# Optimization experiments

Hardware: AMD Instinct MI355X
Metric: run time of the kernel (lower is better)

Reference implementation:

```python
import jax, jax.numpy as jnp
import numpy as np

NUM_HEADS = 32
ROPE_BASE = 10000.0
MASK_NEG = -66504.0  # from (1 - tril) * -66504.0 in the source


def _rotate_half(x):
    d = x.shape[-1] // 2
    return jnp.concatenate([-x[..., d:], x[..., :d]], axis=-1)


def setup_inputs() -> dict:
    key = jax.random.key(0)
    k1, k2, k3, k4 = jax.random.split(key, 4)
    S, B, E = 2048, 2, 2048
    return {
        "hidden_states": jax.random.normal(k1, (S, B, E), dtype=jnp.float32) * 0.02,
        "qkv_w": jax.random.normal(k2, (E, 3 * E), dtype=jnp.float32) * 0.02,
        "qkv_b": jax.random.normal(k3, (3 * E,), dtype=jnp.float32) * 0.02,
        "out_w": jax.random.normal(k4, (E, E), dtype=jnp.float32) * 0.02,
        "out_b": jnp.zeros((E,), dtype=jnp.float32),
    }


def reference(hidden_states, qkv_w, qkv_b, out_w, out_b):
    # seq-first prompt/prefill path of IPEXTransformerAtten
    S, B, E = hidden_states.shape
    H = NUM_HEADS
    D = E // H

    # fused QKV projection (mm_qkv_out)
    qkv = jnp.einsum('sbe,ef->sbf', hidden_states, qkv_w) + qkv_b  # [S,B,3E]
    q, k, v = jnp.split(qkv, 3, axis=-1)
    q = q.reshape(S, B, H, D)
    k = k.reshape(S, B, H, D)
    v = v.reshape(S, B, H, D)

    # rotary embedding (GPT-NeoX style, full head_dim)
    inv_freq = 1.0 / (ROPE_BASE ** (jnp.arange(0, D, 2, dtype=jnp.float32) / D))
    freqs = jnp.arange(S, dtype=jnp.float32)[:, None] * inv_freq  # [S, D/2]
    emb = jnp.concatenate([freqs, freqs], axis=-1)  # [S, D]
    cos = jnp.cos(emb)[:, None, None, :].astype(hidden_states.dtype)
    sin = jnp.sin(emb)[:, None, None, :].astype(hidden_states.dtype)
    q = q * cos + _rotate_half(q) * sin
    k = k * cos + _rotate_half(k) * sin

    # scaled dot-product attention with causal mask
    scale = 1.0 / jnp.sqrt(jnp.array(D, dtype=hidden_states.dtype))
    scores = jnp.einsum('sbhd,tbhd->bhst', q, k) * scale  # [B,H,S,S]
    causal = jnp.tril(jnp.ones((S, S), dtype=scores.dtype))
    scores = scores + (1.0 - causal) * MASK_NEG
    attn = jax.nn.softmax(scores, axis=-1)
    ctx = jnp.einsum('bhst,tbhd->sbhd', attn, v).reshape(S, B, E)

    # output projection
    return jnp.einsum('sbe,ef->sbf', ctx, out_w) + out_b
```

## Files before the change

kernel.cpp:

```cpp
#include <hip/hip_runtime.h>
#include <hip/hip_bf16.h>

#define S_LEN 2048
#define BATCH 2
#define EMB   2048
#define NH    32
#define HD    64
#define M_ROWS (S_LEN * BATCH)
#define QKV_N  (3 * EMB)

typedef short bf16x8 __attribute__((ext_vector_type(8)));
typedef float f32x4  __attribute__((ext_vector_type(4)));

__device__ __forceinline__ unsigned short f2bf(float f) {
  unsigned int u = __float_as_uint(f);
  u += 0x7fffu + ((u >> 16) & 1u);
  return (unsigned short)(u >> 16);
}
__device__ __forceinline__ unsigned int pkbf(float a, float b) {
  __hip_bfloat162 t = __float22bfloat162_rn(float2{a, b});
  return *reinterpret_cast<unsigned int*>(&t);
}
__device__ __forceinline__ void async_copy16(const void* g, void* lds) {
  __builtin_amdgcn_global_load_lds(
      (const __attribute__((address_space(1))) void*)g,
      (__attribute__((address_space(3))) void*)lds, 16, 0, 0);
}

#if __has_builtin(__builtin_amdgcn_exp2f)
#define EXP2F(x) __builtin_amdgcn_exp2f(x)
#else
#define EXP2F(x) __expf((x) * 0.6931471805599453f)
#endif


__global__ __launch_bounds__(256) void cast_to_bf16(
    const float* __restrict__ in, unsigned short* __restrict__ out, int n4) {
  int i = blockIdx.x * 256 + threadIdx.x;
  if (i >= n4) return;
  float4 v = reinterpret_cast<const float4*>(in)[i];
  ushort4 o;
  o.x = f2bf(v.x); o.y = f2bf(v.y); o.z = f2bf(v.z); o.w = f2bf(v.w);
  reinterpret_cast<ushort4*>(out)[i] = o;
}

__global__ __launch_bounds__(256) void transpose_cast2(
    const float* __restrict__ qkv_w, const float* __restrict__ out_w,
    unsigned short* __restrict__ qkvwT, unsigned short* __restrict__ outwT) {
  __shared__ float tile[32][33];
  const int z = blockIdx.z;
  const int C = z ? EMB : QKV_N;
  const int bc = blockIdx.x * 32;
  if (bc >= C) return;
  const float* in = z ? out_w : qkv_w;
  unsigned short* out = z ? outwT : qkvwT;
  const int br = blockIdx.y * 32;
  const int tx = threadIdx.x & 31, ty = threadIdx.x >> 5;
  #pragma unroll
  for (int rr = ty; rr < 32; rr += 8)
    tile[rr][tx] = in[(size_t)(br + rr) * C + bc + tx];
  __syncthreads();
  #pragma unroll
  for (int rr = ty; rr < 32; rr += 8)
    out[(size_t)(bc + rr) * EMB + br + tx] = f2bf(tile[tx][rr]);
}


__global__ __launch_bounds__(256) void gemm_qkv(
    const unsigned short* __restrict__ A,
    const unsigned short* __restrict__ Wt,
    const float* __restrict__ bias,
    unsigned short* __restrict__ Qo,
    unsigned short* __restrict__ Ko,
    unsigned short* __restrict__ Vo) {
  __shared__ __align__(16) unsigned short As[128 * 64];
  __shared__ __align__(16) unsigned short Bs[128 * 64];
  const int tid = threadIdx.x;
  const int n0 = blockIdx.x * 128;
  const int m0 = blockIdx.y * 128;
  const int wave = tid >> 6, lane = tid & 63;
  const int wm = (wave >> 1) * 64, wn = (wave & 1) * 64;
  const int lm = lane & 15, lq = lane >> 4;
  const int K = 2048;

  const int srow = tid >> 3;
  const int gch  = (tid & 7) ^ (srow & 7);
  const unsigned short* Ab = A  + (size_t)(m0 + srow) * K + gch * 8;
  const unsigned short* Bb = Wt + (size_t)(n0 + srow) * K + gch * 8;

  f32x4 acc[4][4] = {};

  for (int k0 = 0; k0 < K; k0 += 64) {
    #pragma unroll
    for (int rep = 0; rep < 4; rep++) {
      async_copy16(Ab + (size_t)rep * 32 * K + k0, As + (size_t)(tid + 256 * rep) * 8);
      async_copy16(Bb + (size_t)rep * 32 * K + k0, Bs + (size_t)(tid + 256 * rep) * 8);
    }
    __syncthreads();
    #pragma unroll
    for (int ks = 0; ks < 2; ks++) {
      bf16x8 a[4], b[4];
      #pragma unroll
      for (int i = 0; i < 4; i++) {
        const int R = wm + i*16 + lm;
        a[i] = *reinterpret_cast<const bf16x8*>(
            As + (size_t)R * 64 + (((ks*4 + lq) ^ (R & 7)) * 8));
      }
      #pragma unroll
      for (int j = 0; j < 4; j++) {
        const int R = wn + j*16 + lm;
        b[j] = *reinterpret_cast<const bf16x8*>(
            Bs + (size_t)R * 64 + (((ks*4 + lq) ^ (R & 7)) * 8));
      }
      #pragma unroll
      for (int i = 0; i < 4; i++)
        #pragma unroll
        for (int j = 0; j < 4; j++)
          acc[i][j] = __builtin_amdgcn_mfma_f32_16x16x32_bf16(a[i], b[j], acc[i][j], 0, 0, 0);
    }
    __syncthreads();
  }

  const int which = n0 >> 11;
  unsigned short* dst = (which == 0) ? Qo : (which == 1) ? Ko : Vo;
  float bv[4];
  #pragma unroll
  for (int j = 0; j < 4; j++) bv[j] = bias[n0 + wn + j*16 + lm];

  if (which < 2) {
    const float osc = (which == 0) ? 0.18033688011112042f : 1.0f;
    #pragma unroll
    for (int j = 0; j < 2; j++) {
      const int n = n0 + wn + j*16 + lm;
      const int e = n & (EMB - 1), h = e >> 6, d = e & 63;
      const float invf = EXP2F((float)d * -0.4152410118609203f);
      #pragma unroll
      for (int i = 0; i < 4; i++) {
        #pragma unroll
        for (int r = 0; r < 4; r++) {
          const int m = m0 + wm + i*16 + lq*4 + r;
          const int s = m >> 1, b = m & 1;
          const float v1 = acc[i][j][r]   + bv[j];
          const float v2 = acc[i][j+2][r] + bv[j+2];
          float sn, cs;
          __sincosf((float)s * invf, &sn, &cs);
          const size_t base = (((size_t)b * NH + h) * S_LEN + s) * HD + d;
          dst[base]      = f2bf((v1 * cs - v2 * sn) * osc);
          dst[base + 32] = f2bf((v2 * cs + v1 * sn) * osc);
        }
      }
    }
  } else {
    #pragma unroll
    for (int j = 0; j < 4; j++) {
      const int n = n0 + wn + j*16 + lm;
      const int e = n & (EMB - 1), h = e >> 6, d = e & 63;
      #pragma unroll
      for (int i = 0; i < 4; i++) {
        #pragma unroll
        for (int r = 0; r < 4; r++) {
          const int m = m0 + wm + i*16 + lq*4 + r;
          const int s = m >> 1, b = m & 1;
          dst[(((size_t)b * NH + h) * S_LEN + s) * HD + d] = f2bf(acc[i][j][r] + bv[j]);
        }
      }
    }
  }
}


__global__ __launch_bounds__(256) void transpose_v(
    const unsigned short* __restrict__ V, unsigned short* __restrict__ VT) {
  __shared__ unsigned short t[64][65];
  const int bh = blockIdx.y;
  const int s0 = blockIdx.x * 64;
  const int tx = threadIdx.x & 63, ty = threadIdx.x >> 6;
  const unsigned short* src = V + ((size_t)bh * S_LEN + s0) * HD;
  #pragma unroll
  for (int r = ty; r < 64; r += 4)
    t[r][tx] = src[(size_t)r * HD + tx];
  __syncthreads();
  unsigned short* dst = VT + (size_t)bh * HD * S_LEN + s0;
  #pragma unroll
  for (int r = ty; r < 64; r += 4)
    dst[(size_t)r * S_LEN + tx] = t[tx][r];
}


__global__ __launch_bounds__(256) void attn_kernel(
    const unsigned short* __restrict__ Q,
    const unsigned short* __restrict__ K,
    const unsigned short* __restrict__ VT,
    unsigned short* __restrict__ ctx) {
  const int bh = blockIdx.x;
  const int p  = blockIdx.y;
  const int tid = threadIdx.x;
  const int wave = tid >> 6, lane = tid & 63;
  const int lm = lane & 15, lq = lane >> 4;
  const int b = bh >> 5, h = bh & 31;
  const char* Qb8 = (const char*)(Q  + (size_t)bh * S_LEN * HD);
  const char* Kb8 = (const char*)(K  + (size_t)bh * S_LEN * HD);
  const char* Vb8 = (const char*)(VT + (size_t)bh * HD * S_LEN);

  __shared__ __align__(16) unsigned short Ks[2][2][64][32];
  __shared__ __align__(16) unsigned short Vs[2][2][64][32];

  const int rA = p * 128 + wave * 32;
  const int rB = (15 - p) * 128 + wave * 32;
  const int nt = ((15 - p) * 128 >> 6) + 2;

  const int srw = tid >> 2, sc16 = (tid & 3) * 16;

  bf16x8 qf[2][2][2];
  #pragma unroll
  for (int s = 0; s < 2; s++) {
    const int rr = s ? rB : rA;
    #pragma unroll
    for (int i = 0; i < 2; i++)
      #pragma unroll
      for (int ks = 0; ks < 2; ks++)
        qf[s][i][ks] = *reinterpret_cast<const bf16x8*>(
            Qb8 + (size_t)(rr + i*16 + lm) * 128 + ks*64 + lq*16);
  }

  f32x4 O[2][2][4] = {};
  float l[2][2] = {};

  {
    char* kd = (char*)&Ks[0][0][0][0];
    char* vd = (char*)&Vs[0][0][0][0];
    async_copy16(Kb8 + (size_t)srw * 128      + sc16, kd        + tid*16);
    async_copy16(Kb8 + (size_t)srw * 128 + 64 + sc16, kd + 4096 + tid*16);
    async_copy16(Vb8 + (size_t)srw * 4096      + sc16, vd        + tid*16);
    async_copy16(Vb8 + (size_t)srw * 4096 + 64 + sc16, vd + 4096 + tid*16);
  }
  __syncthreads();

  for (int t = 0; t < nt; t++) {
    const int t0 = t * 64;
    const int buf = t & 1;

    if (t + 1 < nt) {
      const int t1 = t0 + 64;
      char* kd = (char*)&Ks[buf ^ 1][0][0][0];
      char* vd = (char*)&Vs[buf ^ 1][0][0][0];
      async_copy16(Kb8 + (size_t)(t1 + srw) * 128      + sc16, kd        + tid*16);
      async_copy16(Kb8 + (size_t)(t1 + srw) * 128 + 64 + sc16, kd + 4096 + tid*16);
      async_copy16(Vb8 + (size_t)srw * 4096 + t1*2      + sc16, vd        + tid*16);
      async_copy16(Vb8 + (size_t)srw * 4096 + t1*2 + 64 + sc16, vd + 4096 + tid*16);
    }

    const char* KsB = (const char*)&Ks[buf][0][0][0];
    const char* VsB = (const char*)&Vs[buf][0][0][0];

    #pragma unroll
    for (int s = 0; s < 2; s++) {
      const int rr = s ? rB : rA;
      if (t0 <= rr + 31) {
        const bool clean = (t0 + 63 <= rr);
        int jm[2];
        jm[1] = clean ? 4 : (((rr + 31 - t0) >> 4) + 1);
        jm[0] = clean ? 4 : ((t0 > rr + 15) ? 0 : (((rr + 15 - t0) >> 4) + 1));

        f32x4 sc[2][4] = {};
        #pragma unroll
        for (int ks = 0; ks < 2; ks++) {
          bf16x8 kf[4];
          #pragma unroll
          for (int j = 0; j < 4; j++)
            if (j < jm[1])
              kf[j] = *reinterpret_cast<const bf16x8*>(
                  KsB + ks*4096 + (j*16 + lm)*64 + lq*16);
          #pragma unroll
          for (int i = 0; i < 2; i++)
            #pragma unroll
            for (int j = 0; j < 4; j++)
              if (j < jm[i])
                sc[i][j] = __builtin_amdgcn_mfma_f32_16x16x32_bf16(
                    kf[j], qf[s][i][ks], sc[i][j], 0, 0, 0);
        }

        unsigned int pb[2][2][4];
        #pragma unroll
        for (int i = 0; i < 2; i++) {
          #pragma unroll
          for (int j = 0; j < 4; j++) {
            const int w = j >> 1, rbase = (j & 1) * 2;
            if (j < jm[i]) {
              const bool full = clean || (t0 + j*16 + 15 <= rr + i*16);
              float pe[4];
              #pragma unroll
              for (int r = 0; r < 4; r++) {
                float v = EXP2F(sc[i][j][r]);
                if (!full) {
                  const int tt = t0 + j*16 + lq*4 + r;
                  const int mm = rr + i*16 + lm;
                  v = (tt <= mm) ? v : 0.0f;
                }
                pe[r] = v;
              }
              l[s][i] += (pe[0] + pe[1]) + (pe[2] + pe[3]);
              pb[i][w][rbase]     = pkbf(pe[0], pe[1]);
              pb[i][w][rbase + 1] = pkbf(pe[2], pe[3]);
            } else {
              pb[i][w][rbase] = 0; pb[i][w][rbase + 1] = 0;
            }
          }
        }

        #pragma unroll
        for (int w = 0; w < 2; w++) {
          if (t0 + w*32 <= rr + 31) {
            bf16x8 av[4];
            #pragma unroll
            for (int jj = 0; jj < 4; jj++) {
              const char* vrow = VsB + w*4096 + (jj*16 + lm)*64;
              unsigned long long q0 = *reinterpret_cast<const unsigned long long*>(vrow + lq*8);
              unsigned long long q1 = *reinterpret_cast<const unsigned long long*>(vrow + 32 + lq*8);
              union { unsigned long long q[2]; bf16x8 v; } u;
              u.q[0] = q0; u.q[1] = q1;
              av[jj] = u.v;
            }
            #pragma unroll
            for (int i = 0; i < 2; i++) {
              if (jm[i] > w*2) {
                union { unsigned int u[4]; bf16x8 v; } pu;
                pu.u[0] = pb[i][w][0]; pu.u[1] = pb[i][w][1];
                pu.u[2] = pb[i][w][2]; pu.u[3] = pb[i][w][3];
                #pragma unroll
                for (int jj = 0; jj < 4; jj++)
                  O[s][i][jj] = __builtin_amdgcn_mfma_f32_16x16x32_bf16(
                      av[jj], pu.v, O[s][i][jj], 0, 0, 0);
              }
            }
          }
        }
      }
    }
    __syncthreads();
  }

  #pragma unroll
  for (int s = 0; s < 2; s++) {
    const int rr = s ? rB : rA;
    #pragma unroll
    for (int i = 0; i < 2; i++) {
      float sum = l[s][i];
      sum += __shfl_xor(sum, 16, 64);
      sum += __shfl_xor(sum, 32, 64);
      const float inv = 1.0f / sum;
      const int srow = rr + i*16 + lm;
      #pragma unroll
      for (int jj = 0; jj < 4; jj++) {
        uint2 e;
        e.x = pkbf(O[s][i][jj][0] * inv, O[s][i][jj][1] * inv);
        e.y = pkbf(O[s][i][jj][2] * inv, O[s][i][jj][3] * inv);
        *reinterpret_cast<uint2*>(
            ctx + ((size_t)srow * BATCH + b) * EMB + h*HD + jj*16 + lq*4) = e;
      }
    }
  }
}


__global__ __launch_bounds__(256) void gemm_out(
    const unsigned short* __restrict__ A,
    const unsigned short* __restrict__ Wt,
    const float* __restrict__ bias,
    float* __restrict__ out) {
  __shared__ __align__(16) unsigned short As[2][128 * 64];
  __shared__ __align__(16) unsigned short Bs[2][128 * 64];
  const int tid = threadIdx.x;
  const int n0 = blockIdx.x * 128;
  const int m0 = blockIdx.y * 128;
  const int wave = tid >> 6, lane = tid & 63;
  const int wm = (wave >> 1) * 64, wn = (wave & 1) * 64;
  const int lm = lane & 15, lq = lane >> 4;
  const int K = 2048;

  const int srow = tid >> 3;
  const int gch  = (tid & 7) ^ (srow & 7);
  const unsigned short* Ab = A  + (size_t)(m0 + srow) * K + gch * 8;
  const unsigned short* Bb = Wt + (size_t)(n0 + srow) * K + gch * 8;

  f32x4 acc[4][4] = {};

  #pragma unroll
  for (int rep = 0; rep < 4; rep++) {
    async_copy16(Ab + (size_t)rep * 32 * K, As[0] + (size_t)(tid + 256 * rep) * 8);
    async_copy16(Bb + (size_t)rep * 32 * K, Bs[0] + (size_t)(tid + 256 * rep) * 8);
  }
  __syncthreads();

  for (int kt = 0; kt < 32; kt++) {
    const int buf = kt & 1;
    if (kt + 1 < 32) {
      const int k1 = (kt + 1) * 64;
      #pragma unroll
      for (int rep = 0; rep < 4; rep++) {
        async_copy16(Ab + (size_t)rep * 32 * K + k1, As[buf ^ 1] + (size_t)(tid + 256 * rep) * 8);
        async_copy16(Bb + (size_t)rep * 32 * K + k1, Bs[buf ^ 1] + (size_t)(tid + 256 * rep) * 8);
      }
    }
    #pragma unroll
    for (int ks = 0; ks < 2; ks++) {
      bf16x8 a[4], b[4];
      #pragma unroll
      for (int i = 0; i < 4; i++) {
        const int R = wm + i*16 + lm;
        a[i] = *reinterpret_cast<const bf16x8*>(
            As[buf] + (size_t)R * 64 + (((ks*4 + lq) ^ (R & 7)) * 8));
      }
      #pragma unroll
      for (int j = 0; j < 4; j++) {
        const int R = wn + j*16 + lm;
        b[j] = *reinterpret_cast<const bf16x8*>(
            Bs[buf] + (size_t)R * 64 + (((ks*4 + lq) ^ (R & 7)) * 8));
      }
      #pragma unroll
      for (int i = 0; i < 4; i++)
        #pragma unroll
        for (int j = 0; j < 4; j++)
          acc[i][j] = __builtin_amdgcn_mfma_f32_16x16x32_bf16(a[i], b[j], acc[i][j], 0, 0, 0);
    }
    __syncthreads();
  }

  #pragma unroll
  for (int j = 0; j < 4; j++) {
    const int n = n0 + wn + j*16 + lm;
    const float bv = bias[n];
    #pragma unroll
    for (int i = 0; i < 4; i++) {
      #pragma unroll
      for (int r = 0; r < 4; r++) {
        const int m = m0 + wm + i*16 + lq*4 + r;
        out[(size_t)m * EMB + n] = acc[i][j][r] + bv;
      }
    }
  }
}


extern "C" void kernel_launch(void* const* d_in, const int* in_sizes, int n_in,
                              void* d_out, int out_size, void* d_ws, size_t ws_size,
                              hipStream_t stream) {
  const float* hidden = (const float*)d_in[0];
  const float* qkv_w  = (const float*)d_in[1];
  const float* qkv_b  = (const float*)d_in[2];
  const float* out_w  = (const float*)d_in[3];
  const float* out_b  = (const float*)d_in[4];
  float* out = (float*)d_out;

  unsigned short* ws = (unsigned short*)d_ws;
  unsigned short* hbf   = ws;
  unsigned short* qkvwT = hbf   + (size_t)M_ROWS * EMB;
  unsigned short* outwT = qkvwT + (size_t)QKV_N * EMB;
  unsigned short* Qb    = outwT + (size_t)EMB * EMB;
  unsigned short* Kb    = Qb    + (size_t)64 * S_LEN * HD;
  unsigned short* Vb    = Kb    + (size_t)64 * S_LEN * HD;
  unsigned short* VTb   = Vb    + (size_t)64 * S_LEN * HD;
  unsigned short* ctx   = VTb   + (size_t)64 * S_LEN * HD;

  cast_to_bf16<<<(M_ROWS * EMB / 4) / 256, 256, 0, stream>>>(hidden, hbf, M_ROWS * EMB / 4);
  transpose_cast2<<<dim3(QKV_N / 32, EMB / 32, 2), 256, 0, stream>>>(qkv_w, out_w, qkvwT, outwT);

  gemm_qkv<<<dim3(QKV_N / 128, M_ROWS / 128), 256, 0, stream>>>(hbf, qkvwT, qkv_b, Qb, Kb, Vb);

  transpose_v<<<dim3(S_LEN / 64, 64), 256, 0, stream>>>(Vb, VTb);

  attn_kernel<<<dim3(64, 8), 256, 0, stream>>>(Qb, Kb, VTb, ctx);

  gemm_out<<<dim3(EMB / 128, M_ROWS / 128), 256, 0, stream>>>(ctx, outwT, out_b, out);
}
```

Baseline: 414.2 us.

## Split attention into one-strip blocks, swizzle V in LDS, single-buffer gemm_out

The attention kernel previously paired a short and a long causal query strip in each block for load balance. Now each block handles one strip, with twice as many blocks launched and the longest strips scheduled first. V tiles are XOR-swizzled when copied into LDS, and the read path applies the matching swizzle, to reduce bank conflicts. The output GEMM drops double buffering to cut LDS use, which may raise occupancy but loses overlap of loads with compute. The weight transpose grid is flattened so no blocks launch only to exit early.

```diff
diff --git a/kernel.cpp b/kernel.cpp
--- a/kernel.cpp
+++ b/kernel.cpp
@@ -48,12 +48,12 @@
     const float* __restrict__ qkv_w, const float* __restrict__ out_w,
     unsigned short* __restrict__ qkvwT, unsigned short* __restrict__ outwT) {
   __shared__ float tile[32][33];
-  const int z = blockIdx.z;
-  const int C = z ? EMB : QKV_N;
-  const int bc = blockIdx.x * 32;
-  if (bc >= C) return;
-  const float* in = z ? out_w : qkv_w;
-  unsigned short* out = z ? outwT : qkvwT;
+  const int bx = blockIdx.x;
+  const float* in;
+  unsigned short* out;
+  int C, bc;
+  if (bx < 192) { in = qkv_w; out = qkvwT; C = QKV_N; bc = bx * 32; }
+  else          { in = out_w; out = outwT; C = EMB;   bc = (bx - 192) * 32; }
   const int br = blockIdx.y * 32;
   const int tx = threadIdx.x & 31, ty = threadIdx.x >> 5;
   #pragma unroll
@@ -193,7 +193,7 @@
     const unsigned short* __restrict__ VT,
     unsigned short* __restrict__ ctx) {
   const int bh = blockIdx.x;
-  const int p  = blockIdx.y;
+  const int strip = 15 - blockIdx.y;
   const int tid = threadIdx.x;
   const int wave = tid >> 6, lane = tid & 63;
   const int lm = lane & 15, lq = lane >> 4;
@@ -205,34 +205,31 @@
   __shared__ __align__(16) unsigned short Ks[2][2][64][32];
   __shared__ __align__(16) unsigned short Vs[2][2][64][32];
 
-  const int rA = p * 128 + wave * 32;
-  const int rB = (15 - p) * 128 + wave * 32;
-  const int nt = ((15 - p) * 128 >> 6) + 2;
-
-  const int srw = tid >> 2, sc16 = (tid & 3) * 16;
-
-  bf16x8 qf[2][2][2];
-  #pragma unroll
-  for (int s = 0; s < 2; s++) {
-    const int rr = s ? rB : rA;
-    #pragma unroll
-    for (int i = 0; i < 2; i++)
-      #pragma unroll
-      for (int ks = 0; ks < 2; ks++)
-        qf[s][i][ks] = *reinterpret_cast<const bf16x8*>(
-            Qb8 + (size_t)(rr + i*16 + lm) * 128 + ks*64 + lq*16);
-  }
-
-  f32x4 O[2][2][4] = {};
-  float l[2][2] = {};
+  const int rr = strip * 128 + wave * 32;
+  const int nt = strip * 2 + 2;
+
+  const int srw = tid >> 2;
+  const int kc16 = (tid & 3) * 16;
+  const int vc16 = ((tid & 3) ^ ((srw >> 1) & 3)) * 16;
+
+  bf16x8 qf[2][2];
+  #pragma unroll
+  for (int i = 0; i < 2; i++)
+    #pragma unroll
+    for (int ks = 0; ks < 2; ks++)
+      qf[i][ks] = *reinterpret_cast<const bf16x8*>(
+          Qb8 + (size_t)(rr + i*16 + lm) * 128 + ks*64 + lq*16);
+
+  f32x4 O[2][4] = {};
+  float l[2] = {};
 
   {
     char* kd = (char*)&Ks[0][0][0][0];
     char* vd = (char*)&Vs[0][0][0][0];
-    async_copy16(Kb8 + (size_t)srw * 128      + sc16, kd        + tid*16);
-    async_copy16(Kb8 + (size_t)srw * 128 + 64 + sc16, kd + 4096 + tid*16);
-    async_copy16(Vb8 + (size_t)srw * 4096      + sc16, vd        + tid*16);
-    async_copy16(Vb8 + (size_t)srw * 4096 + 64 + sc16, vd + 4096 + tid*16);
+    async_copy16(Kb8 + (size_t)srw * 128       + kc16, kd        + tid*16);
+    async_copy16(Kb8 + (size_t)srw * 128 + 64  + kc16, kd + 4096 + tid*16);
+    async_copy16(Vb8 + (size_t)srw * 4096      + vc16, vd        + tid*16);
+    async_copy16(Vb8 + (size_t)srw * 4096 + 64 + vc16, vd + 4096 + tid*16);
   }
   __syncthreads();
 
@@ -244,120 +241,114 @@
       const int t1 = t0 + 64;
       char* kd = (char*)&Ks[buf ^ 1][0][0][0];
       char* vd = (char*)&Vs[buf ^ 1][0][0][0];
-      async_copy16(Kb8 + (size_t)(t1 + srw) * 128      + sc16, kd        + tid*16);
-      async_copy16(Kb8 + (size_t)(t1 + srw) * 128 + 64 + sc16, kd + 4096 + tid*16);
-      async_copy16(Vb8 + (size_t)srw * 4096 + t1*2      + sc16, vd        + tid*16);
-      async_copy16(Vb8 + (size_t)srw * 4096 + t1*2 + 64 + sc16, vd + 4096 + tid*16);
+      async_copy16(Kb8 + (size_t)(t1 + srw) * 128       + kc16, kd        + tid*16);
+      async_copy16(Kb8 + (size_t)(t1 + srw) * 128 + 64  + kc16, kd + 4096 + tid*16);
+      async_copy16(Vb8 + (size_t)srw * 4096 + t1*2      + vc16, vd        + tid*16);
+      async_copy16(Vb8 + (size_t)srw * 4096 + t1*2 + 64 + vc16, vd + 4096 + tid*16);
     }
 
     const char* KsB = (const char*)&Ks[buf][0][0][0];
     const char* VsB = (const char*)&Vs[buf][0][0][0];
 
-    #pragma unroll
-    for (int s = 0; s < 2; s++) {
-      const int rr = s ? rB : rA;
-      if (t0 <= rr + 31) {
-        const bool clean = (t0 + 63 <= rr);
-        int jm[2];
-        jm[1] = clean ? 4 : (((rr + 31 - t0) >> 4) + 1);
-        jm[0] = clean ? 4 : ((t0 > rr + 15) ? 0 : (((rr + 15 - t0) >> 4) + 1));
-
-        f32x4 sc[2][4] = {};
-        #pragma unroll
-        for (int ks = 0; ks < 2; ks++) {
-          bf16x8 kf[4];
+    const bool clean = (t0 + 63 <= rr);
+    int jm[2];
+    jm[1] = clean ? 4 : (((rr + 31 - t0) >> 4) + 1);
+    jm[0] = clean ? 4 : ((t0 > rr + 15) ? 0 : (((rr + 15 - t0) >> 4) + 1));
+
+    f32x4 sc[2][4] = {};
+    #pragma unroll
+    for (int ks = 0; ks < 2; ks++) {
+      bf16x8 kf[4];
+      #pragma unroll
+      for (int j = 0; j < 4; j++)
+        if (j < jm[1])
+          kf[j] = *reinterpret_cast<const bf16x8*>(
+              KsB + ks*4096 + (j*16 + lm)*64 + lq*16);
+      #pragma unroll
+      for (int i = 0; i < 2; i++)
+        #pragma unroll
+        for (int j = 0; j < 4; j++)
+          if (j < jm[i])
+            sc[i][j] = __builtin_amdgcn_mfma_f32_16x16x32_bf16(
+                kf[j], qf[i][ks], sc[i][j], 0, 0, 0);
+    }
+
+    unsigned int pb[2][2][4];
+    #pragma unroll
+    for (int i = 0; i < 2; i++) {
+      #pragma unroll
+      for (int j = 0; j < 4; j++) {
+        const int w = j >> 1, rbase = (j & 1) * 2;
+        if (j < jm[i]) {
+          const bool full = clean || (t0 + j*16 + 15 <= rr + i*16);
+          float pe[4];
           #pragma unroll
-          for (int j = 0; j < 4; j++)
-            if (j < jm[1])
-              kf[j] = *reinterpret_cast<const bf16x8*>(
-                  KsB + ks*4096 + (j*16 + lm)*64 + lq*16);
-          #pragma unroll
-          for (int i = 0; i < 2; i++)
+          for (int r = 0; r < 4; r++) {
+            float v = EXP2F(sc[i][j][r]);
+            if (!full) {
+              const int tt = t0 + j*16 + lq*4 + r;
+              const int mm = rr + i*16 + lm;
+              v = (tt <= mm) ? v : 0.0f;
+            }
+            pe[r] = v;
+          }
+          l[i] += (pe[0] + pe[1]) + (pe[2] + pe[3]);
+          pb[i][w][rbase]     = pkbf(pe[0], pe[1]);
+          pb[i][w][rbase + 1] = pkbf(pe[2], pe[3]);
+        } else {
+          pb[i][w][rbase] = 0; pb[i][w][rbase + 1] = 0;
+        }
+      }
+    }
+
+    #pragma unroll
+    for (int w = 0; w < 2; w++) {
+      if (t0 + w*32 <= rr + 31) {
+        bf16x8 av[4];
+        #pragma unroll
+        for (int jj = 0; jj < 4; jj++) {
+          const int row = jj*16 + lm;
+          const char* vrow = VsB + w*4096 + row*64;
+          const int f = ((row >> 1) & 3) << 1;
+          unsigned long long q0 = *reinterpret_cast<const unsigned long long*>(
+              vrow + (lq ^ f) * 8);
+          unsigned long long q1 = *reinterpret_cast<const unsigned long long*>(
+              vrow + ((4 + lq) ^ f) * 8);
+          union { unsigned long long q[2]; bf16x8 v; } u;
+          u.q[0] = q0; u.q[1] = q1;
+          av[jj] = u.v;
+        }
+        #pragma unroll
+        for (int i = 0; i < 2; i++) {
+          if (jm[i] > w*2) {
+            union { unsigned int u[4]; bf16x8 v; } pu;
+            pu.u[0] = pb[i][w][0]; pu.u[1] = pb[i][w][1];
+            pu.u[2] = pb[i][w][2]; pu.u[3] = pb[i][w][3];
             #pragma unroll
-            for (int j = 0; j < 4; j++)
-              if (j < jm[i])
-                sc[i][j] = __builtin_amdgcn_mfma_f32_16x16x32_bf16(
-                    kf[j], qf[s][i][ks], sc[i][j], 0, 0, 0);
-        }
-
-        unsigned int pb[2][2][4];
-        #pragma unroll
-        for (int i = 0; i < 2; i++) {
-          #pragma unroll
-          for (int j = 0; j < 4; j++) {
-            const int w = j >> 1, rbase = (j & 1) * 2;
-            if (j < jm[i]) {
-              const bool full = clean || (t0 + j*16 + 15 <= rr + i*16);
-              float pe[4];
-              #pragma unroll
-              for (int r = 0; r < 4; r++) {
-                float v = EXP2F(sc[i][j][r]);
-                if (!full) {
-                  const int tt = t0 + j*16 + lq*4 + r;
-                  const int mm = rr + i*16 + lm;
-                  v = (tt <= mm) ? v : 0.0f;
-                }
-                pe[r] = v;
-              }
-              l[s][i] += (pe[0] + pe[1]) + (pe[2] + pe[3]);
-              pb[i][w][rbase]     = pkbf(pe[0], pe[1]);
-              pb[i][w][rbase + 1] = pkbf(pe[2], pe[3]);
-            } else {
-              pb[i][w][rbase] = 0; pb[i][w][rbase + 1] = 0;
-            }
+            for (int jj = 0; jj < 4; jj++)
+              O[i][jj] = __builtin_amdgcn_mfma_f32_16x16x32_bf16(
+                  av[jj], pu.v, O[i][jj], 0, 0, 0);
           }
         }
-
-        #pragma unroll
-        for (int w = 0; w < 2; w++) {
-          if (t0 + w*32 <= rr + 31) {
-            bf16x8 av[4];
-            #pragma unroll
-            for (int jj = 0; jj < 4; jj++) {
-              const char* vrow = VsB + w*4096 + (jj*16 + lm)*64;
-              unsigned long long q0 = *reinterpret_cast<const unsigned long long*>(vrow + lq*8);
-              unsigned long long q1 = *reinterpret_cast<const unsigned long long*>(vrow + 32 + lq*8);
-              union { unsigned long long q[2]; bf16x8 v; } u;
-              u.q[0] = q0; u.q[1] = q1;
-              av[jj] = u.v;
-            }
-            #pragma unroll
-            for (int i = 0; i < 2; i++) {
-              if (jm[i] > w*2) {
-                union { unsigned int u[4]; bf16x8 v; } pu;
-                pu.u[0] = pb[i][w][0]; pu.u[1] = pb[i][w][1];
-                pu.u[2] = pb[i][w][2]; pu.u[3] = pb[i][w][3];
-                #pragma unroll
-                for (int jj = 0; jj < 4; jj++)
-                  O[s][i][jj] = __builtin_amdgcn_mfma_f32_16x16x32_bf16(
-                      av[jj], pu.v, O[s][i][jj], 0, 0, 0);
-              }
-            }
-          }
-        }
       }
     }
     __syncthreads();
   }
 
   #pragma unroll
-  for (int s = 0; s < 2; s++) {
-    const int rr = s ? rB : rA;
-    #pragma unroll
-    for (int i = 0; i < 2; i++) {
-      float sum = l[s][i];
-      sum += __shfl_xor(sum, 16, 64);
-      sum += __shfl_xor(sum, 32, 64);
-      const float inv = 1.0f / sum;
-      const int srow = rr + i*16 + lm;
-      #pragma unroll
-      for (int jj = 0; jj < 4; jj++) {
-        uint2 e;
-        e.x = pkbf(O[s][i][jj][0] * inv, O[s][i][jj][1] * inv);
-        e.y = pkbf(O[s][i][jj][2] * inv, O[s][i][jj][3] * inv);
-        *reinterpret_cast<uint2*>(
-            ctx + ((size_t)srow * BATCH + b) * EMB + h*HD + jj*16 + lq*4) = e;
-      }
+  for (int i = 0; i < 2; i++) {
+    float sum = l[i];
+    sum += __shfl_xor(sum, 16, 64);
+    sum += __shfl_xor(sum, 32, 64);
+    const float inv = 1.0f / sum;
+    const int srow = rr + i*16 + lm;
+    #pragma unroll
+    for (int jj = 0; jj < 4; jj++) {
+      uint2 e;
+      e.x = pkbf(O[i][jj][0] * inv, O[i][jj][1] * inv);
+      e.y = pkbf(O[i][jj][2] * inv, O[i][jj][3] * inv);
+      *reinterpret_cast<uint2*>(
+          ctx + ((size_t)srow * BATCH + b) * EMB + h*HD + jj*16 + lq*4) = e;
     }
   }
 }
@@ -368,8 +359,8 @@
     const unsigned short* __restrict__ Wt,
     const float* __restrict__ bias,
     float* __restrict__ out) {
-  __shared__ __align__(16) unsigned short As[2][128 * 64];
-  __shared__ __align__(16) unsigned short Bs[2][128 * 64];
+  __shared__ __align__(16) unsigned short As[128 * 64];
+  __shared__ __align__(16) unsigned short Bs[128 * 64];
   const int tid = threadIdx.x;
   const int n0 = blockIdx.x * 128;
   const int m0 = blockIdx.y * 128;
@@ -385,23 +376,13 @@
 
   f32x4 acc[4][4] = {};
 
-  #pragma unroll
-  for (int rep = 0; rep < 4; rep++) {
-    async_copy16(Ab + (size_t)rep * 32 * K, As[0] + (size_t)(tid + 256 * rep) * 8);
-    async_copy16(Bb + (size_t)rep * 32 * K, Bs[0] + (size_t)(tid + 256 * rep) * 8);
-  }
-  __syncthreads();
-
-  for (int kt = 0; kt < 32; kt++) {
-    const int buf = kt & 1;
-    if (kt + 1 < 32) {
-      const int k1 = (kt + 1) * 64;
-      #pragma unroll
-      for (int rep = 0; rep < 4; rep++) {
-        async_copy16(Ab + (size_t)rep * 32 * K + k1, As[buf ^ 1] + (size_t)(tid + 256 * rep) * 8);
-        async_copy16(Bb + (size_t)rep * 32 * K + k1, Bs[buf ^ 1] + (size_t)(tid + 256 * rep) * 8);
-      }
-    }
+  for (int k0 = 0; k0 < K; k0 += 64) {
+    #pragma unroll
+    for (int rep = 0; rep < 4; rep++) {
+      async_copy16(Ab + (size_t)rep * 32 * K + k0, As + (size_t)(tid + 256 * rep) * 8);
+      async_copy16(Bb + (size_t)rep * 32 * K + k0, Bs + (size_t)(tid + 256 * rep) * 8);
+    }
+    __syncthreads();
     #pragma unroll
     for (int ks = 0; ks < 2; ks++) {
       bf16x8 a[4], b[4];
@@ -409,13 +390,13 @@
       for (int i = 0; i < 4; i++) {
         const int R = wm + i*16 + lm;
         a[i] = *reinterpret_cast<const bf16x8*>(
-            As[buf] + (size_t)R * 64 + (((ks*4 + lq) ^ (R & 7)) * 8));
+            As + (size_t)R * 64 + (((ks*4 + lq) ^ (R & 7)) * 8));
       }
       #pragma unroll
       for (int j = 0; j < 4; j++) {
         const int R = wn + j*16 + lm;
         b[j] = *reinterpret_cast<const bf16x8*>(
-            Bs[buf] + (size_t)R * 64 + (((ks*4 + lq) ^ (R & 7)) * 8));
+            Bs + (size_t)R * 64 + (((ks*4 + lq) ^ (R & 7)) * 8));
       }
       #pragma unroll
       for (int i = 0; i < 4; i++)
@@ -463,13 +444,13 @@
   unsigned short* ctx   = VTb   + (size_t)64 * S_LEN * HD;
 
   cast_to_bf16<<<(M_ROWS * EMB / 4) / 256, 256, 0, stream>>>(hidden, hbf, M_ROWS * EMB / 4);
-  transpose_cast2<<<dim3(QKV_N / 32, EMB / 32, 2), 256, 0, stream>>>(qkv_w, out_w, qkvwT, outwT);
+  transpose_cast2<<<dim3(256, EMB / 32), 256, 0, stream>>>(qkv_w, out_w, qkvwT, outwT);
 
   gemm_qkv<<<dim3(QKV_N / 128, M_ROWS / 128), 256, 0, stream>>>(hbf, qkvwT, qkv_b, Qb, Kb, Vb);
 
   transpose_v<<<dim3(S_LEN / 64, 64), 256, 0, stream>>>(Vb, VTb);
 
-  attn_kernel<<<dim3(64, 8), 256, 0, stream>>>(Qb, Kb, VTb, ctx);
+  attn_kernel<<<dim3(64, 16), 256, 0, stream>>>(Qb, Kb, VTb, ctx);
 
   gemm_out<<<dim3(EMB / 128, M_ROWS / 128), 256, 0, stream>>>(ctx, outwT, out_b, out);
 }
```

Result: faster. 380.6 us (-8.1%).
